# Kernel optimization log

Measured on AMD Instinct MI355X. Metric: run time of the kernel, lower is better.

Reference implementation:

```python
import jax, jax.numpy as jnp
import numpy as np

B, L, D_MODEL, H, D_K, D_V = 64, 52, 4096, 32, 128, 128
NEW_C = D_MODEL // H  # per-head input channel after the (faithful) raw reshape


def setup_inputs() -> dict:
    key = jax.random.key(0)
    ks = jax.random.split(key, 12)
    s = 0.02
    return {
        "Q": jax.random.normal(ks[0], (B, L, D_MODEL), jnp.float32),
        "K": jax.random.normal(ks[1], (B, L, D_MODEL), jnp.float32),
        "V": jax.random.normal(ks[2], (B, L, D_MODEL), jnp.float32),
        "Wq": jax.random.normal(ks[3], (H, NEW_C, D_K), jnp.float32) * s,
        "bq": jnp.zeros((H, D_K), jnp.float32),
        "Wk": jax.random.normal(ks[4], (H, NEW_C, D_K), jnp.float32) * s,
        "bk": jnp.zeros((H, D_K), jnp.float32),
        "Wv": jax.random.normal(ks[5], (H, NEW_C, D_V), jnp.float32) * s,
        "bv": jnp.zeros((H, D_V), jnp.float32),
        "Wo": jax.random.normal(ks[6], (H * D_V, D_MODEL), jnp.float32) * s,
        "bo": jnp.zeros((D_MODEL,), jnp.float32),
    }


def reference(Q, K, V, Wq, bq, Wk, bk, Wv, bv, Wo, bo):
    # Faithful to source: raw reshape (B, L, D) -> (B, H, L, D/H), NOT a channel split.
    def split(x):
        return x.reshape(B, H, L, NEW_C)

    q = jnp.einsum('bhlc,hck->bhlk', split(Q), Wq) + bq[None, :, None, :]  # (B,H,L,D_K)
    k = jnp.einsum('bhlc,hck->bhlk', split(K), Wk) + bk[None, :, None, :]
    v = jnp.einsum('bhlc,hcv->bhlv', split(V), Wv) + bv[None, :, None, :]

    scores = jnp.einsum('bhqk,bhmk->bhqm', q, k) / jnp.sqrt(jnp.asarray(D_K, q.dtype))
    # causal mask: keep j <= i, else -inf (matches the numpy masking loop)
    causal = jnp.tril(jnp.ones((L, L), bool))
    scores = jnp.where(causal[None, None], scores, -jnp.inf)
    attn = jax.nn.softmax(scores, axis=-1)
    o = jnp.einsum('bhqm,bhmv->bhqv', attn, v)  # (B,H,L,D_V)
    o = o.transpose(0, 2, 1, 3).reshape(B, L, H * D_V)  # concat heads on last axis
    # Dropout(0.1) is identity at inference.
    return o @ Wo + bo
```

## Files before the change

### kernel.cpp

```cpp
#include <hip/hip_runtime.h>
#include <hip/hip_bf16.h>

#define B_SZ   64
#define L_SZ   52
#define DMODEL 4096
#define H_SZ   32
#define C_SZ   128
#define DK     128

#define GM 3328
#define GN 4096
#define GK 4096

typedef __bf16 bf16x8 __attribute__((ext_vector_type(8)));
typedef float  f32x4  __attribute__((ext_vector_type(4)));

__device__ __forceinline__ void gload_lds16(const void* g, void* l) {
  __builtin_amdgcn_global_load_lds(
      (__attribute__((address_space(1))) void*)(void*)g,
      (__attribute__((address_space(3))) void*)l, 16, 0, 0);
}

__device__ __forceinline__ unsigned short bfbits(float x) {
  union { __hip_bfloat16 h; unsigned short u; } c;
  c.h = __float2bfloat16(x);
  return c.u;
}

__global__ __launch_bounds__(256) void w3_transpose_kernel(
    const float* __restrict__ Wq, const float* __restrict__ Wk,
    const float* __restrict__ Wv, __hip_bfloat16* __restrict__ WqT,
    __hip_bfloat16* __restrict__ WkT, __hip_bfloat16* __restrict__ WvT) {
  __shared__ float tile[64][65];
  const int bz = blockIdx.z;
  const float* in = (bz < 32 ? Wq : (bz < 64 ? Wk : Wv)) + (size_t)(bz & 31) * 16384;
  __hip_bfloat16* out = (bz < 32 ? WqT : (bz < 64 ? WkT : WvT)) + (size_t)(bz & 31) * 16384;
  const int nt = blockIdx.x, mt = blockIdx.y;
  const int t = threadIdx.x;
  const int r  = t >> 4;
  const int c4 = (t & 15) << 2;
#pragma unroll
  for (int p = 0; p < 4; ++p) {
    const int rr = r + p * 16;
    const float4 v = *(const float4*)(in + (size_t)(mt * 64 + rr) * 128 + nt * 64 + c4);
    tile[rr][c4 + 0] = v.x; tile[rr][c4 + 1] = v.y;
    tile[rr][c4 + 2] = v.z; tile[rr][c4 + 3] = v.w;
  }
  __syncthreads();
#pragma unroll
  for (int p = 0; p < 4; ++p) {
    const int rr = r + p * 16;
    union { __hip_bfloat16 h[4]; ushort4 u; } o4;
#pragma unroll
    for (int e = 0; e < 4; ++e) o4.h[e] = __float2bfloat16(tile[c4 + e][rr]);
    *(ushort4*)(out + (size_t)(nt * 64 + rr) * 128 + mt * 64 + c4) = o4.u;
  }
}

__device__ __forceinline__ void proj_swap136(
    const __hip_bfloat16* __restrict__ xs, const __hip_bfloat16* __restrict__ WT,
    const float* __restrict__ bias, __hip_bfloat16* __restrict__ out,
    int n0, int r16, int kq) {
  f32x4 acc[2][4] = {};
  bf16x8 wf[2][4];
#pragma unroll
  for (int ct = 0; ct < 2; ++ct)
#pragma unroll
    for (int kk = 0; kk < 4; ++kk)
      wf[ct][kk] = *(const bf16x8*)(WT + (n0 + ct * 16 + r16) * 128 + kk * 32 + kq * 8);
#pragma unroll
  for (int kk = 0; kk < 4; ++kk) {
    bf16x8 xf[4];
#pragma unroll
    for (int rt = 0; rt < 4; ++rt) {
      const int row = rt * 16 + r16;
      const int rowc = row < 52 ? row : 51;
      xf[rt] = *(const bf16x8*)(xs + rowc * 136 + kk * 32 + kq * 8);
    }
#pragma unroll
    for (int ct = 0; ct < 2; ++ct)
#pragma unroll
      for (int rt = 0; rt < 4; ++rt)
        acc[ct][rt] = __builtin_amdgcn_mfma_f32_16x16x32_bf16(wf[ct][kk], xf[rt], acc[ct][rt], 0, 0, 0);
  }
#pragma unroll
  for (int ct = 0; ct < 2; ++ct) {
    const int col0 = n0 + ct * 16 + kq * 4;
    const float4 b4 = *(const float4*)(bias + col0);
#pragma unroll
    for (int rt = 0; rt < 4; ++rt) {
      const int row = rt * 16 + r16;
      if (row < 52) {
        ushort4 o;
        o.x = bfbits(acc[ct][rt][0] + b4.x);
        o.y = bfbits(acc[ct][rt][1] + b4.y);
        o.z = bfbits(acc[ct][rt][2] + b4.z);
        o.w = bfbits(acc[ct][rt][3] + b4.w);
        *(ushort4*)(out + row * 136 + col0) = o;
      }
    }
  }
}

__device__ __forceinline__ uint2 shfl64(uint2 v, int lane) {
  uint2 r;
  r.x = (unsigned)__shfl((int)v.x, lane);
  r.y = (unsigned)__shfl((int)v.y, lane);
  return r;
}

__global__ __launch_bounds__(256, 3) void attn_fused_kernel(
    const float* __restrict__ Qin, const float* __restrict__ Kin,
    const float* __restrict__ Vin,
    const __hip_bfloat16* __restrict__ WqT, const float* __restrict__ bq,
    const __hip_bfloat16* __restrict__ WkT, const float* __restrict__ bk,
    const __hip_bfloat16* __restrict__ WvT, const float* __restrict__ bv,
    __hip_bfloat16* __restrict__ Oc,
    const float* __restrict__ Wo, __hip_bfloat16* __restrict__ WoT) {
  __shared__ __align__(16) char lds[42432];
  const int gid = blockIdx.x;
  const int t = threadIdx.x;

  if (gid >= 2048) {
    float* tile = (float*)lds;
    const int bid2 = gid - 2048;
    const int nt = bid2 & 63, mt = bid2 >> 6;
    const int r  = t >> 4;
    const int c4 = (t & 15) << 2;
#pragma unroll
    for (int p = 0; p < 4; ++p) {
      const int rr = r + p * 16;
      const float4 v = *(const float4*)(Wo + (size_t)(mt * 64 + rr) * 4096 + nt * 64 + c4);
      tile[rr * 65 + c4 + 0] = v.x; tile[rr * 65 + c4 + 1] = v.y;
      tile[rr * 65 + c4 + 2] = v.z; tile[rr * 65 + c4 + 3] = v.w;
    }
    __syncthreads();
#pragma unroll
    for (int p = 0; p < 4; ++p) {
      const int rr = r + p * 16;
      union { __hip_bfloat16 h[4]; ushort4 u; } o4;
#pragma unroll
      for (int e = 0; e < 4; ++e) o4.h[e] = __float2bfloat16(tile[(c4 + e) * 65 + rr]);
      *(ushort4*)(WoT + (size_t)(nt * 64 + rr) * 4096 + mt * 64 + c4) = o4.u;
    }
    return;
  }

  __hip_bfloat16* r0 = (__hip_bfloat16*)(lds);
  __hip_bfloat16* r1 = (__hip_bfloat16*)(lds + 14144);
  __hip_bfloat16* r2 = (__hip_bfloat16*)(lds + 28288);
  float*          s_sh = (float*)(lds + 14144);
  __hip_bfloat16* p_sh = r0;

  const int h = gid & 31, bb = gid >> 5;
  const int lane = t & 63;
  const int w = t >> 6;
  const int r16 = lane & 15, kq = lane >> 4;
  const size_t xoff = (size_t)bb * (L_SZ * DMODEL) + (size_t)h * (L_SZ * C_SZ);
  const int n0 = w * 32;

#define LOADR(G, XP)                                                           \
  _Pragma("unroll")                                                            \
  for (int j = 0; j < 7; ++j) {                                                \
    const int idx = t + j * 256;                                               \
    if (idx < 1664)                                                            \
      G[j] = *(const float4*)((XP) + (idx >> 5) * 128 + ((idx & 31) << 2));    \
  }
#define STORER(G, XD)                                                          \
  _Pragma("unroll")                                                            \
  for (int j = 0; j < 7; ++j) {                                                \
    const int idx = t + j * 256;                                               \
    if (idx < 1664) {                                                          \
      ushort4 o;                                                               \
      o.x = bfbits(G[j].x); o.y = bfbits(G[j].y);                              \
      o.z = bfbits(G[j].z); o.w = bfbits(G[j].w);                              \
      *(ushort4*)((XD) + (idx >> 5) * 136 + ((idx & 31) << 2)) = o;            \
    }                                                                          \
  }
  bf16x8 wfv[2][4];
  {
    float4 ga[7], gb[7];
    LOADR(ga, Qin + xoff)
    LOADR(gb, Kin + xoff)
    const __hip_bfloat16* WTv = WvT + (size_t)h * 16384;
#pragma unroll
    for (int ct = 0; ct < 2; ++ct)
#pragma unroll
      for (int kk = 0; kk < 4; ++kk)
        wfv[ct][kk] = *(const bf16x8*)(WTv + (n0 + ct * 16 + r16) * 128 + kk * 32 + kq * 8);
    STORER(ga, r0)
    LOADR(ga, Vin + xoff)
    STORER(gb, r1)
    STORER(ga, r2)
  }
  __syncthreads();

  uint2 vb[4][2];
  {
    f32x4 acc[4][2] = {};
#pragma unroll
    for (int kk = 0; kk < 4; ++kk) {
      bf16x8 a[4];
#pragma unroll
      for (int mt = 0; mt < 4; ++mt) {
        const int row = mt * 16 + r16;
        const int rowc = row < 52 ? row : 51;
        a[mt] = *(const bf16x8*)(r2 + rowc * 136 + kk * 32 + kq * 8);
      }
#pragma unroll
      for (int mt = 0; mt < 4; ++mt)
#pragma unroll
        for (int ct = 0; ct < 2; ++ct)
          acc[mt][ct] = __builtin_amdgcn_mfma_f32_16x16x32_bf16(a[mt], wfv[ct][kk], acc[mt][ct], 0, 0, 0);
    }
#pragma unroll
    for (int ct = 0; ct < 2; ++ct) {
      const float bvv = bv[h * 128 + n0 + ct * 16 + r16];
#pragma unroll
      for (int mt = 0; mt < 4; ++mt) {
        vb[mt][ct].x = (unsigned)bfbits(acc[mt][ct][0] + bvv) |
                       ((unsigned)bfbits(acc[mt][ct][1] + bvv) << 16);
        vb[mt][ct].y = (unsigned)bfbits(acc[mt][ct][2] + bvv) |
                       ((unsigned)bfbits(acc[mt][ct][3] + bvv) << 16);
      }
    }
  }
  __syncthreads();

  proj_swap136(r0, WqT + (size_t)h * 16384, bq + h * 128, r2, n0, r16, kq);
  __syncthreads();

  proj_swap136(r1, WkT + (size_t)h * 16384, bk + h * 128, r0, n0, r16, kq);
  __syncthreads();

  {
    const int nq = w * 16;
    f32x4 sacc[4] = {};
#pragma unroll
    for (int kk = 0; kk < 4; ++kk) {
      const int krow = nq + r16;
      const int krc = krow < 52 ? krow : 51;
      const bf16x8 kf = *(const bf16x8*)(r0 + krc * 136 + kk * 32 + kq * 8);
#pragma unroll
      for (int mt = 0; mt < 4; ++mt) {
        const int qrow = mt * 16 + r16;
        const int qrc = qrow < 52 ? qrow : 51;
        const bf16x8 a = *(const bf16x8*)(r2 + qrc * 136 + kk * 32 + kq * 8);
        sacc[mt] = __builtin_amdgcn_mfma_f32_16x16x32_bf16(a, kf, sacc[mt], 0, 0, 0);
      }
    }
    const float scale = 0.08838834764831845f;
#pragma unroll
    for (int mt = 0; mt < 4; ++mt)
#pragma unroll
      for (int i = 0; i < 4; ++i) {
        const int row = mt * 16 + kq * 4 + i;
        if (row < 52) s_sh[row * 68 + nq + r16] = sacc[mt][i] * scale;
      }
  }
  __syncthreads();

  {
    const int r = t >> 2, qd = t & 3;
    if (r < 52) {
      float v[16];
      float mx = -3e38f;
#pragma unroll
      for (int j4 = 0; j4 < 4; ++j4) {
        const f32x4 s4 = *(const f32x4*)(s_sh + r * 68 + qd * 16 + j4 * 4);
#pragma unroll
        for (int e = 0; e < 4; ++e) {
          const int col = qd * 16 + j4 * 4 + e;
          const float val = (col <= r) ? s4[e] : -3e38f;
          v[j4 * 4 + e] = val;
          mx = fmaxf(mx, val);
        }
      }
      mx = fmaxf(mx, __shfl_xor(mx, 1));
      mx = fmaxf(mx, __shfl_xor(mx, 2));
      float ex[16];
      float sum = 0.f;
#pragma unroll
      for (int j = 0; j < 16; ++j) {
        const int col = qd * 16 + j;
        const float e = (col <= r) ? __expf(v[j] - mx) : 0.f;
        ex[j] = e; sum += e;
      }
      sum += __shfl_xor(sum, 1);
      sum += __shfl_xor(sum, 2);
      const float inv = 1.0f / sum;
      union { __hip_bfloat16 h[8]; uint4 q; } p0, p1;
#pragma unroll
      for (int j = 0; j < 8; ++j) {
        p0.h[j] = __float2bfloat16(ex[j] * inv);
        p1.h[j] = __float2bfloat16(ex[8 + j] * inv);
      }
      *(uint4*)(p_sh + r * 72 + qd * 16)     = p0.q;
      *(uint4*)(p_sh + r * 72 + qd * 16 + 8) = p1.q;
    }
  }
  __syncthreads();

  {
    const int half = (kq >> 1) & 1;
    const int src0 = ((kq & 1) << 5) + r16;
    const int src1 = src0 + 16;
    f32x4 oaccT[2][4] = {};
#pragma unroll
    for (int kk = 0; kk < 2; ++kk) {
      bf16x8 bfr[2];
#pragma unroll
      for (int ct = 0; ct < 2; ++ct) {
        const uint2 a0 = shfl64(vb[2 * kk + 0][ct], src0);
        const uint2 a1 = shfl64(vb[2 * kk + 1][ct], src0);
        const uint2 b0 = shfl64(vb[2 * kk + 0][ct], src1);
        const uint2 b1 = shfl64(vb[2 * kk + 1][ct], src1);
        union { unsigned u[4]; bf16x8 v; } asm_;
        asm_.u[0] = half ? a1.x : a0.x;
        asm_.u[1] = half ? a1.y : a0.y;
        asm_.u[2] = half ? b1.x : b0.x;
        asm_.u[3] = half ? b1.y : b0.y;
        bfr[ct] = asm_.v;
      }
      bf16x8 pf[4];
#pragma unroll
      for (int rt = 0; rt < 4; ++rt) {
        const int prow = rt * 16 + r16;
        const int prc = prow < 52 ? prow : 51;
        pf[rt] = *(const bf16x8*)(p_sh + prc * 72 + kk * 32 + kq * 8);
      }
#pragma unroll
      for (int ct = 0; ct < 2; ++ct)
#pragma unroll
        for (int rt = 0; rt < 4; ++rt)
          oaccT[ct][rt] = __builtin_amdgcn_mfma_f32_16x16x32_bf16(bfr[ct], pf[rt], oaccT[ct][rt], 0, 0, 0);
    }
    const size_t obase = (size_t)bb * 52 * 4096 + (size_t)h * 128;
#pragma unroll
    for (int ct = 0; ct < 2; ++ct) {
      const int col0 = n0 + ct * 16 + kq * 4;
#pragma unroll
      for (int rt = 0; rt < 4; ++rt) {
        const int row = rt * 16 + r16;
        if (row < 52) {
          ushort4 o;
          o.x = bfbits(oaccT[ct][rt][0]);
          o.y = bfbits(oaccT[ct][rt][1]);
          o.z = bfbits(oaccT[ct][rt][2]);
          o.w = bfbits(oaccT[ct][rt][3]);
          *(ushort4*)(Oc + obase + (size_t)row * 4096 + col0) = o;
        }
      }
    }
  }
}

#define STAGE(GBASE, REGOFF, KT, KS, WB) do {                                  \
    const __hip_bfloat16* s_ = (GBASE) + (size_t)(KT) * 64 + (KS) * 32;        \
    char* d_ = (WB) + (REGOFF) + ((KS) ? 16384 : 0) + t * 16;                  \
    gload_lds16(s_, d_);                                                       \
    gload_lds16(s_ + (size_t)128 * GK, d_ + 8192);                             \
  } while (0)

#define MFMA16(MQ, BF)                                                         \
  __builtin_amdgcn_s_setprio(1);                                               \
  _Pragma("unroll")                                                            \
  for (int mf = 0; mf < 4; ++mf)                                               \
    _Pragma("unroll")                                                          \
    for (int nf = 0; nf < 4; ++nf)                                             \
      acc[(MQ) * 4 + mf][nf] = __builtin_amdgcn_mfma_f32_16x16x32_bf16(        \
          BF[nf], af[mf], acc[(MQ) * 4 + mf][nf], 0, 0, 0);                    \
  __builtin_amdgcn_s_setprio(0)

#define READ_AF(RB, KS, MQ)                                                    \
  _Pragma("unroll")                                                            \
  for (int mf = 0; mf < 4; ++mf)                                               \
    af[mf] = *(const bf16x8*)((RB) + (KS) * 16384 + (MQ) * 4096 + aB0 + mf * 1024)

#define READ_BF(RB, BF, KS)                                                    \
  _Pragma("unroll")                                                            \
  for (int nf = 0; nf < 4; ++nf)                                               \
    BF[nf] = *(const bf16x8*)((RB) + 32768 + (KS) * 16384 + bB0 + nf * 1024)

#define KTILE_BODY(KT, RB, OB) do {                                            \
    const int s1 = (KT) + 1 < 64 ? (KT) + 1 : 63;                              \
    const int s2 = (KT) + 2 < 64 ? (KT) + 2 : 63;                              \
    {                                                                          \
      bf16x8 af[4];                                                            \
      READ_AF(RB, 0, 0);                                                       \
      READ_BF(RB, bf0, 0);                                                     \
      STAGE(gA0, 0, s1, 1, OB);                                                \
      __builtin_amdgcn_s_barrier();                                            \
      MFMA16(0, bf0);                                                          \
      __builtin_amdgcn_s_barrier();                                            \
    }                                                                          \
    {                                                                          \
      bf16x8 af[4];                                                            \
      READ_AF(RB, 0, 1);                                                       \
      STAGE(gB0, 32768, s2, 0, RB);                                            \
      __builtin_amdgcn_s_barrier();                                            \
      MFMA16(1, bf0);                                                          \
      __builtin_amdgcn_s_barrier();                                            \
    }                                                                          \
    {                                                                          \
      bf16x8 af[4];                                                            \
      READ_AF(RB, 1, 0);                                                       \
      READ_BF(RB, bf1, 1);                                                     \
      STAGE(gA0, 0, s2, 0, RB);                                                \
      __builtin_amdgcn_s_barrier();                                            \
      MFMA16(0, bf1);                                                          \
      __builtin_amdgcn_s_barrier();                                            \
    }                                                                          \
    {                                                                          \
      bf16x8 af[4];                                                            \
      READ_AF(RB, 1, 1);                                                       \
      STAGE(gB0, 32768, s2, 1, RB);                                            \
      __builtin_amdgcn_s_barrier();                                            \
      MFMA16(1, bf1);                                                          \
      asm volatile("s_waitcnt vmcnt(6)" ::: "memory");                         \
      __builtin_amdgcn_s_barrier();                                            \
    }                                                                          \
  } while (0)

__global__ __launch_bounds__(512, 2) void out_gemm_kernel(
    const __hip_bfloat16* __restrict__ A, const __hip_bfloat16* __restrict__ Bt,
    const float* __restrict__ bias, float* __restrict__ C) {
  __shared__ __align__(16) char lds[131072];

  int bid = blockIdx.x;
  bid = (bid & 7) * 26 + (bid >> 3);
  const int tm = bid >> 4;
  const int tn = bid & 15;

  const int t = threadIdx.x;
  const int w = t >> 6, lane = t & 63;
  const int wm = w >> 2, wn = w & 3;
  const int r16 = lane & 15, kq = lane >> 4;

  const int srow = t >> 2;
  const int sgslot = (t & 3) ^ ((srow >> 1) & 3);
  const __hip_bfloat16* gA0 = A  + (size_t)(tm * 256 + srow) * GK + sgslot * 8;
  const __hip_bfloat16* gB0 = Bt + (size_t)(tn * 256 + srow) * GK + sgslot * 8;

  const int slotr = kq ^ ((r16 >> 1) & 3);
  const int aB0 = (wm * 128 + r16) * 64 + slotr * 16;
  const int bB0 = (wn * 64 + r16) * 64 + slotr * 16;

  f32x4 acc[8][4] = {};
  bf16x8 bf0[4], bf1[4];

  char* const buf0 = lds;
  char* const buf1 = lds + 65536;

  STAGE(gA0, 0,     0, 0, buf0);
  STAGE(gA0, 0,     0, 1, buf0);
  STAGE(gB0, 32768, 0, 0, buf0);
  STAGE(gB0, 32768, 0, 1, buf0);
  STAGE(gB0, 32768, 1, 0, buf1);
  STAGE(gA0, 0,     1, 0, buf1);
  STAGE(gB0, 32768, 1, 1, buf1);
  asm volatile("s_waitcnt vmcnt(6)" ::: "memory");
  __builtin_amdgcn_s_barrier();

#pragma unroll 1
  for (int kt2 = 0; kt2 < 32; ++kt2) {
    const int kt = kt2 * 2;
    KTILE_BODY(kt,     buf0, buf1);
    KTILE_BODY(kt + 1, buf1, buf0);
  }
  asm volatile("s_waitcnt vmcnt(0) lgkmcnt(0)" ::: "memory");

  const int row0 = tm * 256 + wm * 128 + r16;
  const int col0 = tn * 256 + wn * 64 + kq * 4;
  float4 b4[4];
#pragma unroll
  for (int nf = 0; nf < 4; ++nf)
    b4[nf] = *(const float4*)(bias + col0 + nf * 16);
#pragma unroll
  for (int mf = 0; mf < 8; ++mf) {
    const int row = row0 + mf * 16;
#pragma unroll
    for (int nf = 0; nf < 4; ++nf) {
      float4 st;
      st.x = acc[mf][nf][0] + b4[nf].x;
      st.y = acc[mf][nf][1] + b4[nf].y;
      st.z = acc[mf][nf][2] + b4[nf].z;
      st.w = acc[mf][nf][3] + b4[nf].w;
      *(float4*)(C + (size_t)row * GN + col0 + nf * 16) = st;
    }
  }
}

extern "C" void kernel_launch(void* const* d_in, const int* in_sizes, int n_in,
                              void* d_out, int out_size, void* d_ws, size_t ws_size,
                              hipStream_t stream) {
  const float* Q  = (const float*)d_in[0];
  const float* K  = (const float*)d_in[1];
  const float* V  = (const float*)d_in[2];
  const float* Wq = (const float*)d_in[3];
  const float* bq = (const float*)d_in[4];
  const float* Wk = (const float*)d_in[5];
  const float* bk = (const float*)d_in[6];
  const float* Wv = (const float*)d_in[7];
  const float* bv = (const float*)d_in[8];
  const float* Wo = (const float*)d_in[9];
  const float* bo = (const float*)d_in[10];
  float* out = (float*)d_out;

  char* wsb = (char*)d_ws;
  __hip_bfloat16* WoT = (__hip_bfloat16*)wsb;
  __hip_bfloat16* Oc  = (__hip_bfloat16*)(wsb + (size_t)GN * GK * 2);
  __hip_bfloat16* WqT = (__hip_bfloat16*)(wsb + (size_t)GN * GK * 2 + (size_t)GM * GN * 2);
  __hip_bfloat16* WkT = WqT + (size_t)H_SZ * C_SZ * DK;
  __hip_bfloat16* WvT = WkT + (size_t)H_SZ * C_SZ * DK;

  w3_transpose_kernel<<<dim3(2, 2, 96), 256, 0, stream>>>(Wq, Wk, Wv, WqT, WkT, WvT);
  attn_fused_kernel<<<dim3(2048 + 4096), 256, 0, stream>>>(
      Q, K, V, WqT, bq, WkT, bk, WvT, bv, Oc, Wo, WoT);
  out_gemm_kernel<<<dim3(13 * 16), 512, 0, stream>>>(Oc, WoT, bo, out);
}
```

Measured before the change: 185.1 us.

## Load A operand directly from global into registers, keep only B in LDS

```diff
diff --git a/kernel.cpp b/kernel.cpp
--- a/kernel.cpp
+++ b/kernel.cpp
@@ -355,69 +355,48 @@
   }
 }
 
-#define STAGE(GBASE, REGOFF, KT, KS, WB) do {                                  \
-    const __hip_bfloat16* s_ = (GBASE) + (size_t)(KT) * 64 + (KS) * 32;        \
-    char* d_ = (WB) + (REGOFF) + ((KS) ? 16384 : 0) + t * 16;                  \
-    gload_lds16(s_, d_);                                                       \
-    gload_lds16(s_ + (size_t)128 * GK, d_ + 8192);                             \
-  } while (0)
-
-#define MFMA16(MQ, BF)                                                         \
+#define STAGE_B(KT, BUFOFF)                                                    \
+  _Pragma("unroll")                                                            \
+  for (int g = 0; g < 4; ++g)                                                  \
+    gload_lds16(gB0 + (size_t)g * 64 * GK + (size_t)(KT) * 64,                 \
+                lds + (BUFOFF) + g * 8192 + t * 16)
+
+#define ISSUE_AF(DST, KT, KS)                                                  \
+  _Pragma("unroll")                                                            \
+  for (int mf = 0; mf < 8; ++mf)                                               \
+    DST[mf] = *(const bf16x8*)(gA0 + (size_t)mf * 16 * GK + (size_t)(KT) * 64 + (KS) * 32)
+
+#define READ_BFv(BUFOFF, KS)                                                   \
+  _Pragma("unroll")                                                            \
+  for (int nf = 0; nf < 4; ++nf)                                               \
+    bf[nf] = *(const bf16x8*)(lds + (BUFOFF) + (brow + nf * 16) * 128 +        \
+                              slotR[KS] * 16)
+
+#define MFMA32(AF)                                                             \
   __builtin_amdgcn_s_setprio(1);                                               \
   _Pragma("unroll")                                                            \
-  for (int mf = 0; mf < 4; ++mf)                                               \
+  for (int mf = 0; mf < 8; ++mf)                                               \
     _Pragma("unroll")                                                          \
     for (int nf = 0; nf < 4; ++nf)                                             \
-      acc[(MQ) * 4 + mf][nf] = __builtin_amdgcn_mfma_f32_16x16x32_bf16(        \
-          BF[nf], af[mf], acc[(MQ) * 4 + mf][nf], 0, 0, 0);                    \
+      acc[mf][nf] = __builtin_amdgcn_mfma_f32_16x16x32_bf16(                   \
+          bf[nf], AF[mf], acc[mf][nf], 0, 0, 0);                               \
   __builtin_amdgcn_s_setprio(0)
 
-#define READ_AF(RB, KS, MQ)                                                    \
-  _Pragma("unroll")                                                            \
-  for (int mf = 0; mf < 4; ++mf)                                               \
-    af[mf] = *(const bf16x8*)((RB) + (KS) * 16384 + (MQ) * 4096 + aB0 + mf * 1024)
-
-#define READ_BF(RB, BF, KS)                                                    \
-  _Pragma("unroll")                                                            \
-  for (int nf = 0; nf < 4; ++nf)                                               \
-    BF[nf] = *(const bf16x8*)((RB) + 32768 + (KS) * 16384 + bB0 + nf * 1024)
-
-#define KTILE_BODY(KT, RB, OB) do {                                            \
+#define GTILE(KT, BC, BN) do {                                                 \
     const int s1 = (KT) + 1 < 64 ? (KT) + 1 : 63;                              \
-    const int s2 = (KT) + 2 < 64 ? (KT) + 2 : 63;                              \
-    {                                                                          \
-      bf16x8 af[4];                                                            \
-      READ_AF(RB, 0, 0);                                                       \
-      READ_BF(RB, bf0, 0);                                                     \
-      STAGE(gA0, 0, s1, 1, OB);                                                \
-      __builtin_amdgcn_s_barrier();                                            \
-      MFMA16(0, bf0);                                                          \
-      __builtin_amdgcn_s_barrier();                                            \
+    {                                                             \
+      bf16x8 bf[4];                                                            \
+      READ_BFv(BC, 0);                                                         \
+      STAGE_B(s1, BN);                                                         \
+      MFMA32(af0);                                                             \
+      ISSUE_AF(af0, s1, 0);                                                    \
     }                                                                          \
-    {                                                                          \
-      bf16x8 af[4];                                                            \
-      READ_AF(RB, 0, 1);                                                       \
-      STAGE(gB0, 32768, s2, 0, RB);                                            \
-      __builtin_amdgcn_s_barrier();                                            \
-      MFMA16(1, bf0);                                                          \
-      __builtin_amdgcn_s_barrier();                                            \
-    }                                                                          \
-    {                                                                          \
-      bf16x8 af[4];                                                            \
-      READ_AF(RB, 1, 0);                                                       \
-      READ_BF(RB, bf1, 1);                                                     \
-      STAGE(gA0, 0, s2, 0, RB);                                                \
-      __builtin_amdgcn_s_barrier();                                            \
-      MFMA16(0, bf1);                                                          \
-      __builtin_amdgcn_s_barrier();                                            \
-    }                                                                          \
-    {                                                                          \
-      bf16x8 af[4];                                                            \
-      READ_AF(RB, 1, 1);                                                       \
-      STAGE(gB0, 32768, s2, 1, RB);                                            \
-      __builtin_amdgcn_s_barrier();                                            \
-      MFMA16(1, bf1);                                                          \
-      asm volatile("s_waitcnt vmcnt(6)" ::: "memory");                         \
+    {                                                             \
+      bf16x8 bf[4];                                                            \
+      READ_BFv(BC, 1);                                                         \
+      MFMA32(af1);                                                             \
+      ISSUE_AF(af1, s1, 1);                                                    \
+      asm volatile("s_waitcnt vmcnt(16)" ::: "memory");                        \
       __builtin_amdgcn_s_barrier();                                            \
     }                                                                          \
   } while (0)
@@ -425,7 +404,7 @@
 __global__ __launch_bounds__(512, 2) void out_gemm_kernel(
     const __hip_bfloat16* __restrict__ A, const __hip_bfloat16* __restrict__ Bt,
     const float* __restrict__ bias, float* __restrict__ C) {
-  __shared__ __align__(16) char lds[131072];
+  __shared__ __align__(16) char lds[65536];
 
   int bid = blockIdx.x;
   bid = (bid & 7) * 26 + (bid >> 3);
@@ -437,36 +416,29 @@
   const int wm = w >> 2, wn = w & 3;
   const int r16 = lane & 15, kq = lane >> 4;
 
-  const int srow = t >> 2;
-  const int sgslot = (t & 3) ^ ((srow >> 1) & 3);
-  const __hip_bfloat16* gA0 = A  + (size_t)(tm * 256 + srow) * GK + sgslot * 8;
-  const __hip_bfloat16* gB0 = Bt + (size_t)(tn * 256 + srow) * GK + sgslot * 8;
-
-  const int slotr = kq ^ ((r16 >> 1) & 3);
-  const int aB0 = (wm * 128 + r16) * 64 + slotr * 16;
-  const int bB0 = (wn * 64 + r16) * 64 + slotr * 16;
+  const int srow0 = t >> 3;
+  const int gslot = (t & 7) ^ (srow0 & 7);
+  const __hip_bfloat16* gB0 = Bt + (size_t)(tn * 256 + srow0) * GK + gslot * 8;
+
+  const int brow = wn * 64 + r16;
+  const int slotR[2] = { (0 * 4 + kq) ^ (r16 & 7), (1 * 4 + kq) ^ (r16 & 7) };
+
+  const __hip_bfloat16* gA0 = A + (size_t)(tm * 256 + wm * 128 + r16) * GK + kq * 8;
 
   f32x4 acc[8][4] = {};
-  bf16x8 bf0[4], bf1[4];
-
-  char* const buf0 = lds;
-  char* const buf1 = lds + 65536;
-
-  STAGE(gA0, 0,     0, 0, buf0);
-  STAGE(gA0, 0,     0, 1, buf0);
-  STAGE(gB0, 32768, 0, 0, buf0);
-  STAGE(gB0, 32768, 0, 1, buf0);
-  STAGE(gB0, 32768, 1, 0, buf1);
-  STAGE(gA0, 0,     1, 0, buf1);
-  STAGE(gB0, 32768, 1, 1, buf1);
-  asm volatile("s_waitcnt vmcnt(6)" ::: "memory");
+  bf16x8 af0[8], af1[8];
+
+  STAGE_B(0, 0);
+  ISSUE_AF(af0, 0, 0);
+  ISSUE_AF(af1, 0, 1);
+  asm volatile("s_waitcnt vmcnt(16)" ::: "memory");
   __builtin_amdgcn_s_barrier();
 
 #pragma unroll 1
   for (int kt2 = 0; kt2 < 32; ++kt2) {
     const int kt = kt2 * 2;
-    KTILE_BODY(kt,     buf0, buf1);
-    KTILE_BODY(kt + 1, buf1, buf0);
+    GTILE(kt,     0,     32768);
+    GTILE(kt + 1, 32768, 0);
   }
   asm volatile("s_waitcnt vmcnt(0) lgkmcnt(0)" ::: "memory");
 
```

After: 361.4 us. 1.95x slower.
